# Kernel tuning notes

Hardware: AMD Instinct MI355X
Metric: run time of the kernel (lower is better)

Reference implementation:

```python
import jax, jax.numpy as jnp
import numpy as np

N_EDGES = 1_600_000
D_FEAT = 32
N_NODES = 50_000


def setup_inputs() -> dict:
    key = jax.random.key(0)
    k1, k2, k3, k4 = jax.random.split(key, 4)
    m = jax.random.normal(k1, (N_EDGES, D_FEAT), dtype=jnp.float32)
    dst = jax.random.randint(k2, (N_EDGES,), 0, N_NODES, dtype=jnp.int64)
    w = jax.random.normal(k3, (4,), dtype=jnp.float32)
    b = jax.random.normal(k4, (1,), dtype=jnp.float32)
    return {"m": m, "dst": dst, "w": w, "b": b, "n_nodes": N_NODES}


def reference(m, dst, w, b, n_nodes):
    # Four segment reductions edge->node over destination index (copy_e_*)
    s = jax.ops.segment_sum(m, dst, num_segments=n_nodes)            # [N, D]
    mn = jax.ops.segment_min(m, dst, num_segments=n_nodes)
    mx = jax.ops.segment_max(m, dst, num_segments=n_nodes)
    deg = jax.ops.segment_sum(jnp.ones((m.shape[0],), m.dtype), dst,
                              num_segments=n_nodes)                  # [N]
    has = (deg > 0)[:, None]
    # DGL returns 0 for zero-degree nodes
    mn = jnp.where(has, mn, 0.0)
    mx = jnp.where(has, mx, 0.0)
    mean = s / jnp.maximum(deg, 1.0)[:, None]
    stacked = jnp.stack([s, mn, mx, mean], axis=-1)                  # [N, D, 4]
    out = jnp.einsum('ndk,k->nd', stacked, w) + b[0]                 # Dense(4,1) + squeeze
    return out
```

## Files before the change

### kernel.cpp

```cpp
#include <hip/hip_runtime.h>
#include <math.h>

#define D_FEAT 32
#define BSHIFT 5
#define NODES_PER_BKT 32
#define TILE 8192
#define PT 32
#define MAXBKT 2048
#define CAP 2048

__global__ void hist_kernel(const int* __restrict__ dst, int* __restrict__ bucketCount,
                            int E4, int nbucket) {
    __shared__ int h[MAXBKT];
    for (int i = threadIdx.x; i < nbucket; i += 256) h[i] = 0;
    __syncthreads();
    const int4* dst4 = (const int4*)dst;
    int tbase4 = blockIdx.x * (TILE / 4);
    #pragma unroll
    for (int k = 0; k < PT / 4; k++) {
        int i4 = tbase4 + k * 256 + threadIdx.x;
        if (i4 < E4) {
            int4 d = dst4[i4];
            atomicAdd(&h[d.x >> BSHIFT], 1);
            atomicAdd(&h[d.y >> BSHIFT], 1);
            atomicAdd(&h[d.z >> BSHIFT], 1);
            atomicAdd(&h[d.w >> BSHIFT], 1);
        }
    }
    __syncthreads();
    for (int i = threadIdx.x; i < nbucket; i += 256) {
        int c = h[i];
        if (c) atomicAdd(&bucketCount[i], c);
    }
}

__global__ void scan_kernel(const int* __restrict__ bucketCount,
                            int* __restrict__ bucketBase, int* __restrict__ bucketCursor,
                            int nbucket, int E) {
    __shared__ int lds[256];
    int tid = threadIdx.x;
    int vals[8];
    int s = 0;
    #pragma unroll
    for (int k = 0; k < 8; k++) {
        int i = tid * 8 + k;
        vals[k] = (i < nbucket) ? bucketCount[i] : 0;
        s += vals[k];
    }
    lds[tid] = s;
    __syncthreads();
    for (int off = 1; off < 256; off <<= 1) {
        int t = (tid >= off) ? lds[tid - off] : 0;
        __syncthreads();
        lds[tid] += t;
        __syncthreads();
    }
    int run = lds[tid] - s;
    #pragma unroll
    for (int k = 0; k < 8; k++) {
        int i = tid * 8 + k;
        if (i < nbucket) { bucketBase[i] = run; bucketCursor[i] = run; }
        run += vals[k];
    }
    if (tid == 0) bucketBase[nbucket] = E;
}

__global__ void partition_kernel(const int* __restrict__ dst,
                                 int* __restrict__ bucketCursor,
                                 unsigned int* __restrict__ keys,
                                 int E4, int nbucket) {
    __shared__ int h[MAXBKT];
    __shared__ int baseL[MAXBKT];
    int tid = threadIdx.x;
    for (int i = tid; i < nbucket; i += 256) h[i] = 0;
    __syncthreads();
    const int4* dst4 = (const int4*)dst;
    int tbase4 = blockIdx.x * (TILE / 4);
    int pk[PT];
    #pragma unroll
    for (int k = 0; k < PT / 4; k++) {
        int i4 = tbase4 + k * 256 + tid;
        if (i4 < E4) {
            int4 d = dst4[i4];
            int b0 = d.x >> BSHIFT; int r0 = atomicAdd(&h[b0], 1);
            int b1 = d.y >> BSHIFT; int r1 = atomicAdd(&h[b1], 1);
            int b2 = d.z >> BSHIFT; int r2 = atomicAdd(&h[b2], 1);
            int b3 = d.w >> BSHIFT; int r3 = atomicAdd(&h[b3], 1);
            pk[4 * k + 0] = (b0 << 18) | ((d.x & (NODES_PER_BKT - 1)) << 13) | r0;
            pk[4 * k + 1] = (b1 << 18) | ((d.y & (NODES_PER_BKT - 1)) << 13) | r1;
            pk[4 * k + 2] = (b2 << 18) | ((d.z & (NODES_PER_BKT - 1)) << 13) | r2;
            pk[4 * k + 3] = (b3 << 18) | ((d.w & (NODES_PER_BKT - 1)) << 13) | r3;
        } else {
            pk[4 * k + 0] = -1; pk[4 * k + 1] = -1;
            pk[4 * k + 2] = -1; pk[4 * k + 3] = -1;
        }
    }
    __syncthreads();
    for (int i = tid; i < nbucket; i += 256) {
        int c = h[i];
        baseL[i] = c ? atomicAdd(&bucketCursor[i], c) : 0;
    }
    __syncthreads();
    #pragma unroll
    for (int k = 0; k < PT / 4; k++) {
        int i4 = tbase4 + k * 256 + tid;
        int e = i4 * 4;
        #pragma unroll
        for (int l = 0; l < 4; l++) {
            int p = pk[4 * k + l];
            if (p >= 0) {
                int b   = p >> 18;
                int loc = (p >> 13) & (NODES_PER_BKT - 1);
                int r   = p & 8191;
                keys[baseL[b] + r] = ((unsigned)loc << 26) | (unsigned)(e + l);
            }
        }
    }
}

__global__ __launch_bounds__(256) void bucket_gather_kernel(
        const float* __restrict__ m,
        const unsigned int* __restrict__ keys,
        const int* __restrict__ bucketBase,
        const float* __restrict__ w,
        const float* __restrict__ bia,
        float* __restrict__ out, int N) {
    __shared__ unsigned int ukey[CAP];
    __shared__ int seid[CAP];
    __shared__ int nh[NODES_PER_BKT];
    __shared__ int noff[NODES_PER_BKT + 1];
    __shared__ int ncur[NODES_PER_BKT];
    int bkt = blockIdx.x;
    int tid = threadIdx.x;
    int start = bucketBase[bkt];
    int cnt = bucketBase[bkt + 1] - start;
    if (cnt > CAP) cnt = CAP;

    if (tid < NODES_PER_BKT) nh[tid] = 0;
    __syncthreads();
    for (int i = tid; i < cnt; i += 256) {
        unsigned int k = keys[start + i];
        ukey[i] = k;
        atomicAdd(&nh[k >> 26], 1);
    }
    __syncthreads();
    if (tid < NODES_PER_BKT) {
        int v = nh[tid];
        int x = v;
        #pragma unroll
        for (int off = 1; off < NODES_PER_BKT; off <<= 1) {
            int t = __shfl_up(x, off, 64);
            if (tid >= off) x += t;
        }
        noff[tid + 1] = x;
        if (tid == 0) noff[0] = 0;
        ncur[tid] = x - v;
    }
    __syncthreads();
    for (int i = tid; i < cnt; i += 256) {
        unsigned int k = ukey[i];
        int pos = atomicAdd(&ncur[k >> 26], 1);
        seid[pos] = (int)(k & 0x03FFFFFFu);
    }
    __syncthreads();

    int hw = tid >> 5;
    int f  = tid & 31;
    int nodeBase = bkt << BSHIFT;
    float w0 = w[0], w1 = w[1], w2 = w[2], w3 = w[3], bb = bia[0];
    for (int nl = hw; nl < NODES_PER_BKT; nl += 8) {
        int node = nodeBase + nl;
        if (node >= N) break;
        int s0 = noff[nl], e0 = noff[nl + 1];
        int deg = e0 - s0;
        float s = 0.0f, mn = INFINITY, mx = -INFINITY;
        int j = s0;
        for (; j + 8 <= e0; j += 8) {
            float v0 = m[seid[j]     * D_FEAT + f];
            float v1 = m[seid[j + 1] * D_FEAT + f];
            float v2 = m[seid[j + 2] * D_FEAT + f];
            float v3 = m[seid[j + 3] * D_FEAT + f];
            float v4 = m[seid[j + 4] * D_FEAT + f];
            float v5 = m[seid[j + 5] * D_FEAT + f];
            float v6 = m[seid[j + 6] * D_FEAT + f];
            float v7 = m[seid[j + 7] * D_FEAT + f];
            s += v0; mn = fminf(mn, v0); mx = fmaxf(mx, v0);
            s += v1; mn = fminf(mn, v1); mx = fmaxf(mx, v1);
            s += v2; mn = fminf(mn, v2); mx = fmaxf(mx, v2);
            s += v3; mn = fminf(mn, v3); mx = fmaxf(mx, v3);
            s += v4; mn = fminf(mn, v4); mx = fmaxf(mx, v4);
            s += v5; mn = fminf(mn, v5); mx = fmaxf(mx, v5);
            s += v6; mn = fminf(mn, v6); mx = fmaxf(mx, v6);
            s += v7; mn = fminf(mn, v7); mx = fmaxf(mx, v7);
        }
        for (; j < e0; j++) {
            float v = m[seid[j] * D_FEAT + f];
            s += v; mn = fminf(mn, v); mx = fmaxf(mx, v);
        }
        bool has = deg > 0;
        float mean = s / fmaxf((float)deg, 1.0f);
        out[node * D_FEAT + f] = w0 * s + w1 * (has ? mn : 0.0f)
                               + w2 * (has ? mx : 0.0f) + w3 * mean + bb;
    }
}

extern "C" void kernel_launch(void* const* d_in, const int* in_sizes, int n_in,
                              void* d_out, int out_size, void* d_ws, size_t ws_size,
                              hipStream_t stream) {
    const float* m   = (const float*)d_in[0];
    const int*   dst = (const int*)  d_in[1];
    const float* w   = (const float*)d_in[2];
    const float* b   = (const float*)d_in[3];

    int E = in_sizes[0] / D_FEAT;
    int N = out_size    / D_FEAT;
    int E4 = E / 4;
    int nbucket = (N + NODES_PER_BKT - 1) >> BSHIFT;

    int* ws           = (int*)d_ws;
    int* bucketCount  = ws;
    int* bucketBase   = bucketCount + MAXBKT;
    int* bucketCursor = bucketBase + MAXBKT + 1;
    unsigned int* keys = (unsigned int*)(bucketCursor + MAXBKT);

    int nTiles = (E + TILE - 1) / TILE;

    hipMemsetAsync(bucketCount, 0, MAXBKT * sizeof(int), stream);
    hipLaunchKernelGGL(hist_kernel, dim3(nTiles), dim3(256), 0, stream,
                       dst, bucketCount, E4, nbucket);
    hipLaunchKernelGGL(scan_kernel, dim3(1), dim3(256), 0, stream,
                       bucketCount, bucketBase, bucketCursor, nbucket, E);
    hipLaunchKernelGGL(partition_kernel, dim3(nTiles), dim3(256), 0, stream,
                       dst, bucketCursor, keys, E4, nbucket);
    hipLaunchKernelGGL(bucket_gather_kernel, dim3(nbucket), dim3(256), 0, stream,
                       m, keys, bucketBase, w, b, (float*)d_out, N);
}
```

Measured before the change: 336.6 us.

## Replace bucketed partition with per-node CSR build and float4 gather

Swaps the two-level bucket partition (block-local histograms plus per-bucket local sort) for a direct per-node CSR. It uses global atomic histograms, a single-block scan over all nodes, and atomic placement of edge ids. The gather kernel now processes 8 nodes per block. Each wavefront reads float4 rows with 8 edges in parallel and combines partial results with shuffle reductions. This removes the in-block sort, but it adds many contended global atomics and a slow single-block 50k scan. It also truncates edges when a group holds more than 640, and edge order within a node becomes nondeterministic.

```diff
diff --git a/kernel.cpp b/kernel.cpp
--- a/kernel.cpp
+++ b/kernel.cpp
@@ -2,205 +2,147 @@
 #include <math.h>
 
 #define D_FEAT 32
-#define BSHIFT 5
-#define NODES_PER_BKT 32
-#define TILE 8192
-#define PT 32
-#define MAXBKT 2048
-#define CAP 2048
+#define NCAP 50048
+#define GSZ 8
+#define CAP 640
+#define SCAN_T 1024
 
-__global__ void hist_kernel(const int* __restrict__ dst, int* __restrict__ bucketCount,
-                            int E4, int nbucket) {
-    __shared__ int h[MAXBKT];
-    for (int i = threadIdx.x; i < nbucket; i += 256) h[i] = 0;
-    __syncthreads();
+__global__ __launch_bounds__(256) void hist_kernel(const int* __restrict__ dst,
+                                                   int* __restrict__ nodeCount, int E) {
+    int gtid = blockIdx.x * 256 + threadIdx.x;
+    int gthreads = gridDim.x * 256;
+    int E4 = E >> 2;
     const int4* dst4 = (const int4*)dst;
-    int tbase4 = blockIdx.x * (TILE / 4);
-    #pragma unroll
-    for (int k = 0; k < PT / 4; k++) {
-        int i4 = tbase4 + k * 256 + threadIdx.x;
-        if (i4 < E4) {
-            int4 d = dst4[i4];
-            atomicAdd(&h[d.x >> BSHIFT], 1);
-            atomicAdd(&h[d.y >> BSHIFT], 1);
-            atomicAdd(&h[d.z >> BSHIFT], 1);
-            atomicAdd(&h[d.w >> BSHIFT], 1);
-        }
+    for (int i = gtid; i < E4; i += gthreads) {
+        int4 d = dst4[i];
+        atomicAdd(&nodeCount[d.x], 1);
+        atomicAdd(&nodeCount[d.y], 1);
+        atomicAdd(&nodeCount[d.z], 1);
+        atomicAdd(&nodeCount[d.w], 1);
     }
-    __syncthreads();
-    for (int i = threadIdx.x; i < nbucket; i += 256) {
-        int c = h[i];
-        if (c) atomicAdd(&bucketCount[i], c);
-    }
+    for (int e = (E4 << 2) + gtid; e < E; e += gthreads)
+        atomicAdd(&nodeCount[dst[e]], 1);
 }
 
-__global__ void scan_kernel(const int* __restrict__ bucketCount,
-                            int* __restrict__ bucketBase, int* __restrict__ bucketCursor,
-                            int nbucket, int E) {
-    __shared__ int lds[256];
+__global__ __launch_bounds__(SCAN_T) void scan_kernel(const int* __restrict__ nodeCount,
+                                                      int* __restrict__ nodeBase,
+                                                      int* __restrict__ nodeCursor, int N) {
+    __shared__ int lds[SCAN_T];
     int tid = threadIdx.x;
-    int vals[8];
+    int total = N + 1;
+    int chunk = (total + SCAN_T - 1) / SCAN_T;
+    int lo = tid * chunk;
+    int hi = lo + chunk; if (hi > total) hi = total;
     int s = 0;
-    #pragma unroll
-    for (int k = 0; k < 8; k++) {
-        int i = tid * 8 + k;
-        vals[k] = (i < nbucket) ? bucketCount[i] : 0;
-        s += vals[k];
-    }
+    for (int i = lo; i < hi; i++) s += nodeCount[i];
     lds[tid] = s;
     __syncthreads();
-    for (int off = 1; off < 256; off <<= 1) {
+    for (int off = 1; off < SCAN_T; off <<= 1) {
         int t = (tid >= off) ? lds[tid - off] : 0;
         __syncthreads();
         lds[tid] += t;
         __syncthreads();
     }
     int run = lds[tid] - s;
-    #pragma unroll
-    for (int k = 0; k < 8; k++) {
-        int i = tid * 8 + k;
-        if (i < nbucket) { bucketBase[i] = run; bucketCursor[i] = run; }
-        run += vals[k];
-    }
-    if (tid == 0) bucketBase[nbucket] = E;
-}
-
-__global__ void partition_kernel(const int* __restrict__ dst,
-                                 int* __restrict__ bucketCursor,
-                                 unsigned int* __restrict__ keys,
-                                 int E4, int nbucket) {
-    __shared__ int h[MAXBKT];
-    __shared__ int baseL[MAXBKT];
-    int tid = threadIdx.x;
-    for (int i = tid; i < nbucket; i += 256) h[i] = 0;
-    __syncthreads();
-    const int4* dst4 = (const int4*)dst;
-    int tbase4 = blockIdx.x * (TILE / 4);
-    int pk[PT];
-    #pragma unroll
-    for (int k = 0; k < PT / 4; k++) {
-        int i4 = tbase4 + k * 256 + tid;
-        if (i4 < E4) {
-            int4 d = dst4[i4];
-            int b0 = d.x >> BSHIFT; int r0 = atomicAdd(&h[b0], 1);
-            int b1 = d.y >> BSHIFT; int r1 = atomicAdd(&h[b1], 1);
-            int b2 = d.z >> BSHIFT; int r2 = atomicAdd(&h[b2], 1);
-            int b3 = d.w >> BSHIFT; int r3 = atomicAdd(&h[b3], 1);
-            pk[4 * k + 0] = (b0 << 18) | ((d.x & (NODES_PER_BKT - 1)) << 13) | r0;
-            pk[4 * k + 1] = (b1 << 18) | ((d.y & (NODES_PER_BKT - 1)) << 13) | r1;
-            pk[4 * k + 2] = (b2 << 18) | ((d.z & (NODES_PER_BKT - 1)) << 13) | r2;
-            pk[4 * k + 3] = (b3 << 18) | ((d.w & (NODES_PER_BKT - 1)) << 13) | r3;
-        } else {
-            pk[4 * k + 0] = -1; pk[4 * k + 1] = -1;
-            pk[4 * k + 2] = -1; pk[4 * k + 3] = -1;
-        }
-    }
-    __syncthreads();
-    for (int i = tid; i < nbucket; i += 256) {
-        int c = h[i];
-        baseL[i] = c ? atomicAdd(&bucketCursor[i], c) : 0;
-    }
-    __syncthreads();
-    #pragma unroll
-    for (int k = 0; k < PT / 4; k++) {
-        int i4 = tbase4 + k * 256 + tid;
-        int e = i4 * 4;
-        #pragma unroll
-        for (int l = 0; l < 4; l++) {
-            int p = pk[4 * k + l];
-            if (p >= 0) {
-                int b   = p >> 18;
-                int loc = (p >> 13) & (NODES_PER_BKT - 1);
-                int r   = p & 8191;
-                keys[baseL[b] + r] = ((unsigned)loc << 26) | (unsigned)(e + l);
-            }
-        }
+    for (int i = lo; i < hi; i++) {
+        nodeBase[i] = run;
+        nodeCursor[i] = run;
+        run += nodeCount[i];
     }
 }
 
-__global__ __launch_bounds__(256) void bucket_gather_kernel(
+__global__ __launch_bounds__(256) void place_kernel(const int* __restrict__ dst,
+                                                    int* __restrict__ nodeCursor,
+                                                    int* __restrict__ keys, int E) {
+    int gtid = blockIdx.x * 256 + threadIdx.x;
+    int gthreads = gridDim.x * 256;
+    int E4 = E >> 2;
+    const int4* dst4 = (const int4*)dst;
+    for (int i = gtid; i < E4; i += gthreads) {
+        int4 d = dst4[i];
+        int e = i << 2;
+        int r0 = atomicAdd(&nodeCursor[d.x], 1); keys[r0] = e;
+        int r1 = atomicAdd(&nodeCursor[d.y], 1); keys[r1] = e + 1;
+        int r2 = atomicAdd(&nodeCursor[d.z], 1); keys[r2] = e + 2;
+        int r3 = atomicAdd(&nodeCursor[d.w], 1); keys[r3] = e + 3;
+    }
+    for (int e = (E4 << 2) + gtid; e < E; e += gthreads) {
+        int r = atomicAdd(&nodeCursor[dst[e]], 1); keys[r] = e;
+    }
+}
+
+__global__ __launch_bounds__(256) void gather_kernel(
         const float* __restrict__ m,
-        const unsigned int* __restrict__ keys,
-        const int* __restrict__ bucketBase,
+        const int* __restrict__ keys,
+        const int* __restrict__ nodeBase,
         const float* __restrict__ w,
         const float* __restrict__ bia,
         float* __restrict__ out, int N) {
-    __shared__ unsigned int ukey[CAP];
-    __shared__ int seid[CAP];
-    __shared__ int nh[NODES_PER_BKT];
-    __shared__ int noff[NODES_PER_BKT + 1];
-    __shared__ int ncur[NODES_PER_BKT];
-    int bkt = blockIdx.x;
-    int tid = threadIdx.x;
-    int start = bucketBase[bkt];
-    int cnt = bucketBase[bkt + 1] - start;
-    if (cnt > CAP) cnt = CAP;
+    __shared__ int seidS[CAP];
+    __shared__ int noffS[GSZ + 1];
+    const int g = blockIdx.x;
+    const int tid = threadIdx.x;
 
-    if (tid < NODES_PER_BKT) nh[tid] = 0;
-    __syncthreads();
-    for (int i = tid; i < cnt; i += 256) {
-        unsigned int k = keys[start + i];
-        ukey[i] = k;
-        atomicAdd(&nh[k >> 26], 1);
+    if (tid < GSZ + 1) {
+        int n = g * GSZ + tid;
+        if (n > N) n = N;
+        noffS[tid] = nodeBase[n];
     }
     __syncthreads();
-    if (tid < NODES_PER_BKT) {
-        int v = nh[tid];
-        int x = v;
-        #pragma unroll
-        for (int off = 1; off < NODES_PER_BKT; off <<= 1) {
-            int t = __shfl_up(x, off, 64);
-            if (tid >= off) x += t;
-        }
-        noff[tid + 1] = x;
-        if (tid == 0) noff[0] = 0;
-        ncur[tid] = x - v;
-    }
-    __syncthreads();
-    for (int i = tid; i < cnt; i += 256) {
-        unsigned int k = ukey[i];
-        int pos = atomicAdd(&ncur[k >> 26], 1);
-        seid[pos] = (int)(k & 0x03FFFFFFu);
-    }
+    const int gs = noffS[0];
+    int cnt = noffS[GSZ] - gs;
+    if (cnt > CAP) cnt = CAP;
+    for (int i = tid; i < cnt; i += 256) seidS[i] = keys[gs + i];
     __syncthreads();
 
-    int hw = tid >> 5;
-    int f  = tid & 31;
-    int nodeBase = bkt << BSHIFT;
-    float w0 = w[0], w1 = w[1], w2 = w[2], w3 = w[3], bb = bia[0];
-    for (int nl = hw; nl < NODES_PER_BKT; nl += 8) {
-        int node = nodeBase + nl;
+    const float w0 = w[0], w1 = w[1], w2 = w[2], w3 = w[3], bb = bia[0];
+    const int lane = tid & 63;
+    const int wv = tid >> 6;
+    const int fo = lane & 7;
+    const int rs = lane >> 3;
+
+    for (int nl = wv; nl < GSZ; nl += 4) {
+        int node = g * GSZ + nl;
         if (node >= N) break;
-        int s0 = noff[nl], e0 = noff[nl + 1];
+        int s0 = noffS[nl] - gs;     if (s0 > cnt) s0 = cnt;
+        int e0 = noffS[nl + 1] - gs; if (e0 > cnt) e0 = cnt;
         int deg = e0 - s0;
-        float s = 0.0f, mn = INFINITY, mx = -INFINITY;
-        int j = s0;
-        for (; j + 8 <= e0; j += 8) {
-            float v0 = m[seid[j]     * D_FEAT + f];
-            float v1 = m[seid[j + 1] * D_FEAT + f];
-            float v2 = m[seid[j + 2] * D_FEAT + f];
-            float v3 = m[seid[j + 3] * D_FEAT + f];
-            float v4 = m[seid[j + 4] * D_FEAT + f];
-            float v5 = m[seid[j + 5] * D_FEAT + f];
-            float v6 = m[seid[j + 6] * D_FEAT + f];
-            float v7 = m[seid[j + 7] * D_FEAT + f];
-            s += v0; mn = fminf(mn, v0); mx = fmaxf(mx, v0);
-            s += v1; mn = fminf(mn, v1); mx = fmaxf(mx, v1);
-            s += v2; mn = fminf(mn, v2); mx = fmaxf(mx, v2);
-            s += v3; mn = fminf(mn, v3); mx = fmaxf(mx, v3);
-            s += v4; mn = fminf(mn, v4); mx = fmaxf(mx, v4);
-            s += v5; mn = fminf(mn, v5); mx = fmaxf(mx, v5);
-            s += v6; mn = fminf(mn, v6); mx = fmaxf(mx, v6);
-            s += v7; mn = fminf(mn, v7); mx = fmaxf(mx, v7);
+        float sa0 = 0.f, sa1 = 0.f, sa2 = 0.f, sa3 = 0.f;
+        float mn0 = INFINITY, mn1 = INFINITY, mn2 = INFINITY, mn3 = INFINITY;
+        float mx0 = -INFINITY, mx1 = -INFINITY, mx2 = -INFINITY, mx3 = -INFINITY;
+        for (int j = s0 + rs; j < e0; j += 8) {
+            int eid = seidS[j];
+            const float4 v = *(const float4*)&m[eid * D_FEAT + (fo << 2)];
+            sa0 += v.x; mn0 = fminf(mn0, v.x); mx0 = fmaxf(mx0, v.x);
+            sa1 += v.y; mn1 = fminf(mn1, v.y); mx1 = fmaxf(mx1, v.y);
+            sa2 += v.z; mn2 = fminf(mn2, v.z); mx2 = fmaxf(mx2, v.z);
+            sa3 += v.w; mn3 = fminf(mn3, v.w); mx3 = fmaxf(mx3, v.w);
         }
-        for (; j < e0; j++) {
-            float v = m[seid[j] * D_FEAT + f];
-            s += v; mn = fminf(mn, v); mx = fmaxf(mx, v);
+        #pragma unroll
+        for (int mask = 8; mask <= 32; mask <<= 1) {
+            sa0 += __shfl_xor(sa0, mask, 64);
+            sa1 += __shfl_xor(sa1, mask, 64);
+            sa2 += __shfl_xor(sa2, mask, 64);
+            sa3 += __shfl_xor(sa3, mask, 64);
+            mn0 = fminf(mn0, __shfl_xor(mn0, mask, 64));
+            mn1 = fminf(mn1, __shfl_xor(mn1, mask, 64));
+            mn2 = fminf(mn2, __shfl_xor(mn2, mask, 64));
+            mn3 = fminf(mn3, __shfl_xor(mn3, mask, 64));
+            mx0 = fmaxf(mx0, __shfl_xor(mx0, mask, 64));
+            mx1 = fmaxf(mx1, __shfl_xor(mx1, mask, 64));
+            mx2 = fmaxf(mx2, __shfl_xor(mx2, mask, 64));
+            mx3 = fmaxf(mx3, __shfl_xor(mx3, mask, 64));
         }
-        bool has = deg > 0;
-        float mean = s / fmaxf((float)deg, 1.0f);
-        out[node * D_FEAT + f] = w0 * s + w1 * (has ? mn : 0.0f)
-                               + w2 * (has ? mx : 0.0f) + w3 * mean + bb;
+        if (rs == 0) {
+            bool has = deg > 0;
+            float inv = 1.0f / fmaxf((float)deg, 1.0f);
+            float4 o;
+            o.x = w0 * sa0 + w1 * (has ? mn0 : 0.f) + w2 * (has ? mx0 : 0.f) + w3 * (sa0 * inv) + bb;
+            o.y = w0 * sa1 + w1 * (has ? mn1 : 0.f) + w2 * (has ? mx1 : 0.f) + w3 * (sa1 * inv) + bb;
+            o.z = w0 * sa2 + w1 * (has ? mn2 : 0.f) + w2 * (has ? mx2 : 0.f) + w3 * (sa2 * inv) + bb;
+            o.w = w0 * sa3 + w1 * (has ? mn3 : 0.f) + w2 * (has ? mx3 : 0.f) + w3 * (sa3 * inv) + bb;
+            *(float4*)&out[node * D_FEAT + (fo << 2)] = o;
+        }
     }
 }
 
@@ -211,27 +153,28 @@
     const int*   dst = (const int*)  d_in[1];
     const float* w   = (const float*)d_in[2];
     const float* b   = (const float*)d_in[3];
+    float* outp = (float*)d_out;
 
     int E = in_sizes[0] / D_FEAT;
     int N = out_size    / D_FEAT;
-    int E4 = E / 4;
-    int nbucket = (N + NODES_PER_BKT - 1) >> BSHIFT;
 
-    int* ws           = (int*)d_ws;
-    int* bucketCount  = ws;
-    int* bucketBase   = bucketCount + MAXBKT;
-    int* bucketCursor = bucketBase + MAXBKT + 1;
-    unsigned int* keys = (unsigned int*)(bucketCursor + MAXBKT);
+    int* ws = (int*)d_ws;
+    int* nodeCount  = ws;
+    int* nodeBase   = nodeCount  + NCAP;
+    int* nodeCursor = nodeBase   + NCAP;
+    int* keys       = nodeCursor + NCAP;
 
-    int nTiles = (E + TILE - 1) / TILE;
+    hipMemsetAsync(nodeCount, 0, NCAP * sizeof(int), stream);
 
-    hipMemsetAsync(bucketCount, 0, MAXBKT * sizeof(int), stream);
-    hipLaunchKernelGGL(hist_kernel, dim3(nTiles), dim3(256), 0, stream,
-                       dst, bucketCount, E4, nbucket);
-    hipLaunchKernelGGL(scan_kernel, dim3(1), dim3(256), 0, stream,
-                       bucketCount, bucketBase, bucketCursor, nbucket, E);
-    hipLaunchKernelGGL(partition_kernel, dim3(nTiles), dim3(256), 0, stream,
-                       dst, bucketCursor, keys, E4, nbucket);
-    hipLaunchKernelGGL(bucket_gather_kernel, dim3(nbucket), dim3(256), 0, stream,
-                       m, keys, bucketBase, w, b, (float*)d_out, N);
+    int nEdgeBlocks = (E / 4 + 255) / 256;
+    int nGather = (N + GSZ - 1) / GSZ;
+
+    hipLaunchKernelGGL(hist_kernel, dim3(nEdgeBlocks), dim3(256), 0, stream,
+                       dst, nodeCount, E);
+    hipLaunchKernelGGL(scan_kernel, dim3(1), dim3(SCAN_T), 0, stream,
+                       nodeCount, nodeBase, nodeCursor, N);
+    hipLaunchKernelGGL(place_kernel, dim3(nEdgeBlocks), dim3(256), 0, stream,
+                       dst, nodeCursor, keys, E);
+    hipLaunchKernelGGL(gather_kernel, dim3(nGather), dim3(256), 0, stream,
+                       m, keys, nodeBase, w, b, outp, N);
 }
```

After: 597.8 us. 77.6% more time.
